# Optimization experiments

Hardware: AMD Instinct MI355X
Metric: run time of the kernel (lower is better)

Reference implementation:

```python
import jax, jax.numpy as jnp
import numpy as np

BINS = 256
MAXV = float(2 ** 14 - 1)
LAP_K = jnp.array([[0.0, 1.0, 0.0], [1.0, -4.0, 1.0], [0.0, 1.0, 0.0]], jnp.float32).reshape(1, 1, 3, 3)


def _soft_hist_entropy(flat):
    # flat: (B, N) in arbitrary range; per-image min-max normalize to [0,1]
    fmin = jnp.min(flat, axis=1, keepdims=True)
    fmax = jnp.max(flat, axis=1, keepdims=True)
    rng = fmax - fmin
    rng = jnp.where(rng == 0, jnp.ones_like(rng), rng)
    x = jnp.clip((flat - fmin) / rng, 0.0, 1.0)
    # Triangular soft-histogram weights clamp(1-|x-c_k|/bw, 0) are nonzero for at
    # most the 2 bins adjacent to x, so scatter-add instead of a (B,N,BINS) tensor.
    p = x * BINS - 0.5            # position in bin-center coordinates
    i0 = jnp.floor(p)
    w1 = p - i0                   # weight on bin i0+1
    w0 = 1.0 - w1                 # weight on bin i0
    i0i = i0.astype(jnp.int32)
    i1i = i0i + 1
    v0 = (i0i >= 0) & (i0i < BINS)
    v1 = (i1i >= 0) & (i1i < BINS)

    def hist_one(idx0, idx1, a0, a1, m0, m1):
        h = jnp.zeros((BINS,), flat.dtype)
        h = h.at[jnp.clip(idx0, 0, BINS - 1)].add(jnp.where(m0, a0, 0.0))
        h = h.at[jnp.clip(idx1, 0, BINS - 1)].add(jnp.where(m1, a1, 0.0))
        return h

    hist = jax.vmap(hist_one)(i0i, i1i, w0, w1, v0, v1)  # (B, BINS)
    hist = hist / (jnp.sum(hist, axis=1, keepdims=True) + 1e-10)
    ent = -jnp.sum(hist * jnp.log2(hist + 1e-10), axis=1)
    return ent / jnp.float32(np.log2(BINS))


def _extract_features(image):
    # normalize 14-bit input to [0,1] iff values exceed 1 (matches torch branch)
    image = jnp.where(jnp.max(image) > 1.0, image / MAXV, image)
    B = image.shape[0]
    flat = image.reshape(B, -1)
    variance = jnp.var(flat, axis=1, ddof=1)   # torch.var is unbiased
    mn = jnp.min(flat, axis=1)
    mx = jnp.max(flat, axis=1)
    ent = _soft_hist_entropy(flat)
    lap = jax.lax.conv_general_dilated(
        image, LAP_K, window_strides=(1, 1), padding=[(1, 1), (1, 1)],
        dimension_numbers=('NCHW', 'OIHW', 'NCHW'))
    lap_var = jnp.var(lap.reshape(B, -1), axis=1, ddof=1)
    return jnp.stack([variance, mn, mx, ent, lap_var], axis=1)  # (B, 5)


def setup_inputs() -> dict:
    key = jax.random.key(0)
    ks = jax.random.split(key, 4)
    image = jax.random.uniform(ks[0], (16, 1, 1024, 1280), jnp.float32) * MAXV
    # Kaiming normal fan_in (relu): std = sqrt(2 / fan_in); biases zero
    W1 = jax.random.normal(ks[1], (64, 5), jnp.float32) * np.float32(np.sqrt(2.0 / 5))
    W2 = jax.random.normal(ks[2], (64, 64), jnp.float32) * np.float32(np.sqrt(2.0 / 64))
    W3 = jax.random.normal(ks[3], (3, 64), jnp.float32) * np.float32(np.sqrt(2.0 / 64))
    return {
        'image': image,
        'W1': W1, 'b1': jnp.zeros((64,), jnp.float32),
        'W2': W2, 'b2': jnp.zeros((64,), jnp.float32),
        'W3': W3, 'b3': jnp.zeros((3,), jnp.float32),
    }


def reference(image, W1, b1, W2, b2, W3, b3):
    feats = _extract_features(image)                       # (B, 5)
    h = jax.nn.relu(feats @ W1.T + b1)
    h = jax.nn.relu(h @ W2.T + b2)
    logits = h @ W3.T + b3                                  # (B, 3)
    probs = jax.nn.softmax(logits, axis=1)
    class_ids = jnp.argmax(probs, axis=1)
    return class_ids, probs, feats
```

## Files before the change

kernel.cpp:

```cpp
#include <hip/hip_runtime.h>
#include <cfloat>
#include <math.h>

#define IMG_B 16
#define IMG_H 1024
#define IMG_W 1280
#define NPIX (IMG_H * IMG_W)
#define BINS 256
#define SLICES 64
#define NBLK (IMG_B * SLICES)
#define F4_PER_SLICE (16 * IMG_W / 4)

__device__ __forceinline__ unsigned encf(float f) {
    unsigned u = __float_as_uint(f);
    return (u >> 31) ? ~u : (u | 0x80000000u);
}
__device__ __forceinline__ float decf(unsigned u) {
    unsigned b = (u & 0x80000000u) ? (u & 0x7fffffffu) : ~u;
    return __uint_as_float(b);
}


__global__ __launch_bounds__(256) void k_minmax(const float* __restrict__ img,
                                                uint2* __restrict__ mmp) {
    const int blk = blockIdx.x;
    const int tid = threadIdx.x;
    const int lane = tid & 63, wv = tid >> 6;

    const float4* p = (const float4*)img + (size_t)blk * F4_PER_SLICE;
    float fmn = FLT_MAX, fmx = -FLT_MAX;
    #pragma unroll 4
    for (int k = 0; k < 20; ++k) {
        float4 v = p[tid + k * 256];
        fmn = fminf(fmn, fminf(fminf(v.x, v.y), fminf(v.z, v.w)));
        fmx = fmaxf(fmx, fmaxf(fmaxf(v.x, v.y), fmaxf(v.z, v.w)));
    }
    for (int o = 32; o; o >>= 1) {
        fmn = fminf(fmn, __shfl_down(fmn, (unsigned)o, 64));
        fmx = fmaxf(fmx, __shfl_down(fmx, (unsigned)o, 64));
    }
    __shared__ float rmn[4], rmx[4];
    if (lane == 0) { rmn[wv] = fmn; rmx[wv] = fmx; }
    __syncthreads();
    if (tid == 0) {
        float mn = fminf(fminf(rmn[0], rmn[1]), fminf(rmn[2], rmn[3]));
        float mx = fmaxf(fmaxf(rmx[0], rmx[1]), fmaxf(rmx[2], rmx[3]));
        mmp[blk] = make_uint2(encf(mn), encf(mx));
    }
}

__global__ __launch_bounds__(256) void k_main(const float* __restrict__ img,
                                              const uint2* __restrict__ mmp,
                                              double* __restrict__ mom,
                                              unsigned* __restrict__ bhist) {
    const int blk = blockIdx.x;
    const int tid = threadIdx.x;
    const int b   = blk >> 6;
    const int sl  = blk & 63;
    const int lane = tid & 63, wv = tid >> 6;

    __shared__ unsigned long long lh64[BINS + 1];
    __shared__ float sh_ab[2];
    __shared__ float swred[4][4];

    if (tid < 64) {
        uint2 e = mmp[b * 64 + tid];
        unsigned emn = e.x, emx = e.y;
        for (int o = 32; o; o >>= 1) {
            emn = min(emn, (unsigned)__shfl_down(emn, (unsigned)o, 64));
            emx = max(emx, (unsigned)__shfl_down(emx, (unsigned)o, 64));
        }
        if (tid == 0) {
            float fmn = decf(emn), fmx = decf(emx);
            float rng = fmx - fmn;
            if (rng == 0.f) rng = 1.f;
            float a = 256.f / rng;
            float bb = -fmn * a - 0.5f;
            sh_ab[0] = a; sh_ab[1] = bb;
        }
    }
    lh64[tid] = 0ull;
    if (tid == 0) lh64[BINS] = 0ull;
    __syncthreads();

    const float a = sh_ab[0], bb = sh_ab[1];
    const float* base = img + (size_t)b * NPIX;
    const int r0 = sl * 16;

    float fs = 0.f, fs2 = 0.f, fls = 0.f, fls2 = 0.f;

    #pragma unroll 2
    for (int k = 0; k < 20; ++k) {
        int i   = tid + k * 256;
        int ri  = i / 320;
        int c   = i - ri * 320;
        int r   = r0 + ri;
        const float* rowf = base + (size_t)r * IMG_W;
        float4 m = ((const float4*)rowf)[c];
        float4 up = make_float4(0.f, 0.f, 0.f, 0.f);
        float4 dn = make_float4(0.f, 0.f, 0.f, 0.f);
        if (r > 0)          up = ((const float4*)(rowf - IMG_W))[c];
        if (r < IMG_H - 1)  dn = ((const float4*)(rowf + IMG_W))[c];
        float lft = (c > 0)   ? rowf[4 * c - 1] : 0.f;
        float rgt = (c < 319) ? rowf[4 * c + 4] : 0.f;

        fs  += (m.x + m.y) + (m.z + m.w);
        fs2 += (m.x * m.x + m.y * m.y) + (m.z * m.z + m.w * m.w);

        float l0 = up.x + dn.x + lft + m.y - 4.f * m.x;
        float l1 = up.y + dn.y + m.x + m.z - 4.f * m.y;
        float l2 = up.z + dn.z + m.y + m.w - 4.f * m.z;
        float l3 = up.w + dn.w + m.z + rgt - 4.f * m.w;
        fls  += (l0 + l1) + (l2 + l3);
        fls2 += (l0 * l0 + l1 * l1) + (l2 * l2 + l3 * l3);

        #pragma unroll
        for (int j = 0; j < 4; ++j) {
            float vv = (j == 0) ? m.x : (j == 1) ? m.y : (j == 2) ? m.z : m.w;
            float pp = fminf(fmaxf(vv * a + bb, -0.5f), 255.5f);
            float fi = floorf(pp);
            int   i0 = (int)fi;
            unsigned w1q = (unsigned)((pp - fi) * 65536.f + 0.5f);
            atomicAdd(&lh64[i0 + 1], 0x100000000ull + (unsigned long long)w1q);
        }
    }

    for (int o = 32; o; o >>= 1) {
        fs   += __shfl_down(fs,   (unsigned)o, 64);
        fs2  += __shfl_down(fs2,  (unsigned)o, 64);
        fls  += __shfl_down(fls,  (unsigned)o, 64);
        fls2 += __shfl_down(fls2, (unsigned)o, 64);
    }
    if (lane == 0) {
        swred[0][wv] = fs;  swred[1][wv] = fs2;
        swred[2][wv] = fls; swred[3][wv] = fls2;
    }
    __syncthreads();

    if (tid == 0) {
        double S   = (double)swred[0][0] + (double)swred[0][1] + (double)swred[0][2] + (double)swred[0][3];
        double S2  = (double)swred[1][0] + (double)swred[1][1] + (double)swred[1][2] + (double)swred[1][3];
        double LS  = (double)swred[2][0] + (double)swred[2][1] + (double)swred[2][2] + (double)swred[2][3];
        double LS2 = (double)swred[3][0] + (double)swred[3][1] + (double)swred[3][2] + (double)swred[3][3];
        mom[blk * 4 + 0] = S;  mom[blk * 4 + 1] = S2;
        mom[blk * 4 + 2] = LS; mom[blk * 4 + 3] = LS2;
    }

    unsigned long long a0 = lh64[tid];
    unsigned long long a1 = lh64[tid + 1];
    unsigned long long h  = ((a1 >> 32) << 16) - (a1 & 0xffffffffull) + (a0 & 0xffffffffull);
    bhist[blk * BINS + tid] = (unsigned)h;
}

__global__ __launch_bounds__(256) void k_final(
    const unsigned* __restrict__ bhist, const double* __restrict__ mom,
    const uint2* __restrict__ mmp,
    const float* __restrict__ W1, const float* __restrict__ b1,
    const float* __restrict__ W2, const float* __restrict__ b2,
    const float* __restrict__ W3, const float* __restrict__ b3,
    float* __restrict__ out)
{
    const int ib = blockIdx.x;
    const int tid = threadIdx.x;
    const int lane = tid & 63, wv = tid >> 6;

    __shared__ double dred[4];
    __shared__ float  fred[4];
    __shared__ double smom[4];
    __shared__ unsigned smm2[2];
    __shared__ unsigned sgm[4];
    __shared__ float f5[5], h1[64], h2[64], lg[3];

    double h = 0.0;
    for (int s = 0; s < 64; ++s)
        h += (double)bhist[(ib * 64 + s) * BINS + tid];

    double tot = h;
    for (int o = 32; o; o >>= 1) tot += __shfl_down(tot, (unsigned)o, 64);
    if (lane == 0) dred[wv] = tot;
    __syncthreads();
    tot = dred[0] + dred[1] + dred[2] + dred[3];

    double hv = h * (1.0 / 65536.0);
    double tv = tot * (1.0 / 65536.0);
    float hn = (float)(hv / (tv + 1e-10));
    float ce = hn * log2f(hn + 1e-10f);
    for (int o = 32; o; o >>= 1) ce += __shfl_down(ce, (unsigned)o, 64);
    if (lane == 0) fred[wv] = ce;

    if (tid < 64) {
        double q0 = mom[(ib * 64 + tid) * 4 + 0];
        double q1 = mom[(ib * 64 + tid) * 4 + 1];
        double q2 = mom[(ib * 64 + tid) * 4 + 2];
        double q3 = mom[(ib * 64 + tid) * 4 + 3];
        uint2 e = mmp[ib * 64 + tid];
        unsigned emn = e.x, emx = e.y;
        for (int o = 32; o; o >>= 1) {
            q0 += __shfl_down(q0, (unsigned)o, 64);
            q1 += __shfl_down(q1, (unsigned)o, 64);
            q2 += __shfl_down(q2, (unsigned)o, 64);
            q3 += __shfl_down(q3, (unsigned)o, 64);
            emn = min(emn, (unsigned)__shfl_down(emn, (unsigned)o, 64));
            emx = max(emx, (unsigned)__shfl_down(emx, (unsigned)o, 64));
        }
        if (tid == 0) {
            smom[0] = q0; smom[1] = q1; smom[2] = q2; smom[3] = q3;
            smm2[0] = emn; smm2[1] = emx;
        }
    }
    {
        unsigned g = max(max(mmp[tid].y, mmp[256 + tid].y),
                         max(mmp[512 + tid].y, mmp[768 + tid].y));
        for (int o = 32; o; o >>= 1)
            g = max(g, (unsigned)__shfl_down(g, (unsigned)o, 64));
        if (lane == 0) sgm[wv] = g;
    }
    __syncthreads();

    if (tid == 0) {
        float ent = -(fred[0] + fred[1] + fred[2] + fred[3]) / 8.f;
        float gmax = decf(max(max(sgm[0], sgm[1]), max(sgm[2], sgm[3])));
        float sc = (gmax > 1.f) ? (1.f / 16383.f) : 1.f;
        double N = (double)NPIX;
        double S = smom[0], S2 = smom[1], LS = smom[2], LS2 = smom[3];
        double sc2 = (double)sc * (double)sc;
        float var  = (float)((S2  - S  * S  / N) / (N - 1.0) * sc2);
        float lvar = (float)((LS2 - LS * LS / N) / (N - 1.0) * sc2);
        float mn = decf(smm2[0]) * sc;
        float mx = decf(smm2[1]) * sc;
        float* fo = out + 64 + ib * 5;
        fo[0] = var; fo[1] = mn; fo[2] = mx; fo[3] = ent; fo[4] = lvar;
        f5[0] = var; f5[1] = mn; f5[2] = mx; f5[3] = ent; f5[4] = lvar;
    }
    __syncthreads();

    if (tid < 64) {
        float aa = b1[tid];
        #pragma unroll
        for (int k = 0; k < 5; ++k) aa += W1[tid * 5 + k] * f5[k];
        h1[tid] = fmaxf(aa, 0.f);
    }
    __syncthreads();
    if (tid < 64) {
        float a2 = b2[tid];
        #pragma unroll
        for (int k = 0; k < 64; ++k) a2 += W2[tid * 64 + k] * h1[k];
        h2[tid] = fmaxf(a2, 0.f);
    }
    __syncthreads();
    if (tid < 3) {
        float a3 = b3[tid];
        #pragma unroll
        for (int k = 0; k < 64; ++k) a3 += W3[tid * 64 + k] * h2[k];
        lg[tid] = a3;
    }
    __syncthreads();
    if (tid == 0) {
        float m = fmaxf(lg[0], fmaxf(lg[1], lg[2]));
        float e0 = expf(lg[0] - m), e1 = expf(lg[1] - m), e2 = expf(lg[2] - m);
        float inv = 1.f / (e0 + e1 + e2);
        float p0 = e0 * inv, p1 = e1 * inv, p2 = e2 * inv;
        out[16 + ib * 3 + 0] = p0;
        out[16 + ib * 3 + 1] = p1;
        out[16 + ib * 3 + 2] = p2;
        int cid = 0; float bm = p0;
        if (p1 > bm) { bm = p1; cid = 1; }
        if (p2 > bm) { bm = p2; cid = 2; }
        out[ib] = (float)cid;
    }
}

extern "C" void kernel_launch(void* const* d_in, const int* in_sizes, int n_in,
                              void* d_out, int out_size, void* d_ws, size_t ws_size,
                              hipStream_t stream) {
    const float* img = (const float*)d_in[0];
    const float* W1  = (const float*)d_in[1];
    const float* b1  = (const float*)d_in[2];
    const float* W2  = (const float*)d_in[3];
    const float* b2  = (const float*)d_in[4];
    const float* W3  = (const float*)d_in[5];
    const float* b3  = (const float*)d_in[6];
    float* out = (float*)d_out;

    char* ws = (char*)d_ws;
    uint2*    mmp   = (uint2*)ws;
    double*   mom   = (double*)(ws + 8192);
    unsigned* bhist = (unsigned*)(ws + 40960);

    k_minmax<<<NBLK, 256, 0, stream>>>(img, mmp);
    k_main  <<<NBLK, 256, 0, stream>>>(img, mmp, mom, bhist);
    k_final <<<IMG_B, 256, 0, stream>>>(bhist, mom, mmp,
                                        W1, b1, W2, b2, W3, b3, out);
}
```

Baseline: 156.2 us.

## Fuse final reduction kernel into main kernel via last-block-done counter

Removes the separate k_final launch. Each k_main block publishes its histogram and moments with agent-scope atomic stores, then bumps a per-image counter. The last block for each image runs the final entropy, moments and MLP computation. This cuts one kernel launch and the gap between kernels, in exchange for an atomic counter, fences and some extra register and shared-memory pressure in k_main.

```diff
diff --git a/kernel.cpp b/kernel.cpp
--- a/kernel.cpp
+++ b/kernel.cpp
@@ -19,13 +19,30 @@
     unsigned b = (u & 0x80000000u) ? (u & 0x7fffffffu) : ~u;
     return __uint_as_float(b);
 }
+__device__ __forceinline__ void st_u32(unsigned* p, unsigned v) {
+    __hip_atomic_store(p, v, __ATOMIC_RELAXED, __HIP_MEMORY_SCOPE_AGENT);
+}
+__device__ __forceinline__ unsigned ld_u32(const unsigned* p) {
+    return __hip_atomic_load(p, __ATOMIC_RELAXED, __HIP_MEMORY_SCOPE_AGENT);
+}
+__device__ __forceinline__ void st_f64(double* p, double v) {
+    __hip_atomic_store((unsigned long long*)p, (unsigned long long)__double_as_longlong(v),
+                       __ATOMIC_RELAXED, __HIP_MEMORY_SCOPE_AGENT);
+}
+__device__ __forceinline__ double ld_f64(const double* p) {
+    return __longlong_as_double((long long)__hip_atomic_load(
+        (const unsigned long long*)p, __ATOMIC_RELAXED, __HIP_MEMORY_SCOPE_AGENT));
+}
 
 
 __global__ __launch_bounds__(256) void k_minmax(const float* __restrict__ img,
-                                                uint2* __restrict__ mmp) {
+                                                uint2* __restrict__ mmp,
+                                                unsigned* __restrict__ cnt) {
     const int blk = blockIdx.x;
     const int tid = threadIdx.x;
     const int lane = tid & 63, wv = tid >> 6;
+
+    if (blk < IMG_B && tid == 0) cnt[blk] = 0u;
 
     const float4* p = (const float4*)img + (size_t)blk * F4_PER_SLICE;
     float fmn = FLT_MAX, fmx = -FLT_MAX;
@@ -49,10 +66,15 @@
     }
 }
 
-__global__ __launch_bounds__(256) void k_main(const float* __restrict__ img,
-                                              const uint2* __restrict__ mmp,
-                                              double* __restrict__ mom,
-                                              unsigned* __restrict__ bhist) {
+__global__ __launch_bounds__(256) void k_main(
+    const float* __restrict__ img, const uint2* __restrict__ mmp,
+    double* __restrict__ mom, unsigned* __restrict__ bhist,
+    unsigned* __restrict__ cnt,
+    const float* __restrict__ W1, const float* __restrict__ b1,
+    const float* __restrict__ W2, const float* __restrict__ b2,
+    const float* __restrict__ W3, const float* __restrict__ b3,
+    float* __restrict__ out)
+{
     const int blk = blockIdx.x;
     const int tid = threadIdx.x;
     const int b   = blk >> 6;
@@ -62,6 +84,7 @@
     __shared__ unsigned long long lh64[BINS + 1];
     __shared__ float sh_ab[2];
     __shared__ float swred[4][4];
+    __shared__ unsigned slast;
 
     if (tid < 64) {
         uint2 e = mmp[b * 64 + tid];
@@ -142,27 +165,27 @@
         double S2  = (double)swred[1][0] + (double)swred[1][1] + (double)swred[1][2] + (double)swred[1][3];
         double LS  = (double)swred[2][0] + (double)swred[2][1] + (double)swred[2][2] + (double)swred[2][3];
         double LS2 = (double)swred[3][0] + (double)swred[3][1] + (double)swred[3][2] + (double)swred[3][3];
-        mom[blk * 4 + 0] = S;  mom[blk * 4 + 1] = S2;
-        mom[blk * 4 + 2] = LS; mom[blk * 4 + 3] = LS2;
-    }
-
-    unsigned long long a0 = lh64[tid];
-    unsigned long long a1 = lh64[tid + 1];
-    unsigned long long h  = ((a1 >> 32) << 16) - (a1 & 0xffffffffull) + (a0 & 0xffffffffull);
-    bhist[blk * BINS + tid] = (unsigned)h;
-}
-
-__global__ __launch_bounds__(256) void k_final(
-    const unsigned* __restrict__ bhist, const double* __restrict__ mom,
-    const uint2* __restrict__ mmp,
-    const float* __restrict__ W1, const float* __restrict__ b1,
-    const float* __restrict__ W2, const float* __restrict__ b2,
-    const float* __restrict__ W3, const float* __restrict__ b3,
-    float* __restrict__ out)
-{
-    const int ib = blockIdx.x;
-    const int tid = threadIdx.x;
-    const int lane = tid & 63, wv = tid >> 6;
+        st_f64(&mom[blk * 4 + 0], S);  st_f64(&mom[blk * 4 + 1], S2);
+        st_f64(&mom[blk * 4 + 2], LS); st_f64(&mom[blk * 4 + 3], LS2);
+    }
+
+    {
+        unsigned long long a0 = lh64[tid];
+        unsigned long long a1 = lh64[tid + 1];
+        unsigned long long h  = ((a1 >> 32) << 16) - (a1 & 0xffffffffull) + (a0 & 0xffffffffull);
+        st_u32(&bhist[blk * BINS + tid], (unsigned)h);
+    }
+
+    __threadfence();
+    __syncthreads();
+    if (tid == 0)
+        slast = (__hip_atomic_fetch_add(&cnt[b], 1u, __ATOMIC_ACQ_REL,
+                                        __HIP_MEMORY_SCOPE_AGENT) == 63u) ? 1u : 0u;
+    __syncthreads();
+    if (!slast) return;
+    __threadfence();
+
+    const int ib = b;
 
     __shared__ double dred[4];
     __shared__ float  fred[4];
@@ -173,7 +196,7 @@
 
     double h = 0.0;
     for (int s = 0; s < 64; ++s)
-        h += (double)bhist[(ib * 64 + s) * BINS + tid];
+        h += (double)ld_u32(&bhist[(ib * 64 + s) * BINS + tid]);
 
     double tot = h;
     for (int o = 32; o; o >>= 1) tot += __shfl_down(tot, (unsigned)o, 64);
@@ -189,10 +212,10 @@
     if (lane == 0) fred[wv] = ce;
 
     if (tid < 64) {
-        double q0 = mom[(ib * 64 + tid) * 4 + 0];
-        double q1 = mom[(ib * 64 + tid) * 4 + 1];
-        double q2 = mom[(ib * 64 + tid) * 4 + 2];
-        double q3 = mom[(ib * 64 + tid) * 4 + 3];
+        double q0 = ld_f64(&mom[(ib * 64 + tid) * 4 + 0]);
+        double q1 = ld_f64(&mom[(ib * 64 + tid) * 4 + 1]);
+        double q2 = ld_f64(&mom[(ib * 64 + tid) * 4 + 2]);
+        double q3 = ld_f64(&mom[(ib * 64 + tid) * 4 + 3]);
         uint2 e = mmp[ib * 64 + tid];
         unsigned emn = e.x, emx = e.y;
         for (int o = 32; o; o >>= 1) {
@@ -286,9 +309,9 @@
     uint2*    mmp   = (uint2*)ws;
     double*   mom   = (double*)(ws + 8192);
     unsigned* bhist = (unsigned*)(ws + 40960);
-
-    k_minmax<<<NBLK, 256, 0, stream>>>(img, mmp);
-    k_main  <<<NBLK, 256, 0, stream>>>(img, mmp, mom, bhist);
-    k_final <<<IMG_B, 256, 0, stream>>>(bhist, mom, mmp,
-                                        W1, b1, W2, b2, W3, b3, out);
-}
+    unsigned* cnt   = (unsigned*)(ws + 40960 + (size_t)NBLK * BINS * 4);
+
+    k_minmax<<<NBLK, 256, 0, stream>>>(img, mmp, cnt);
+    k_main  <<<NBLK, 256, 0, stream>>>(img, mmp, mom, bhist, cnt,
+                                       W1, b1, W2, b2, W3, b3, out);
+}
```

New measurement: 246.5 us. +57.8%, slower.
